# Kernel optimization log

Measured on AMD Instinct MI355X. Metric: run time of the kernel, lower is better.

The kernel has to match this reference:

```python
import jax, jax.numpy as jnp
import numpy as np

NU, B, N, D = 3, 16, 1024, 256  # n_utils, batch, tokens per util, embed dim


def l2norm(x, axis=-1, eps=1e-12):
    # F.normalize over channel dim: x / max(||x||_2, eps)
    n = jnp.linalg.norm(x, axis=axis, keepdims=True)
    return x / jnp.maximum(n, eps)


def setup_inputs() -> dict:
    key = jax.random.key(0)
    ks = jax.random.split(key, 20)
    s = 0.05
    return {
        "u0": jax.random.normal(ks[0], (B, N, D), jnp.float32),
        "u1": jax.random.normal(ks[1], (B, N, D), jnp.float32),
        "u2": jax.random.normal(ks[2], (B, N, D), jnp.float32),
        # Unary per util: embed Conv1d(D,D,1), feature_reduce Conv1d(D,1,1)
        "Wu": jax.random.normal(ks[3], (NU, D, D), jnp.float32) * s,
        "bu": jax.random.normal(ks[4], (NU, D), jnp.float32) * s,
        "wr": jax.random.normal(ks[5], (NU, D), jnp.float32) * s,
        "br": jax.random.normal(ks[6], (NU,), jnp.float32) * s,
        # Self Pairwise per util: embed_X, embed_Y Conv1d(D,D,1)
        "Wsx": jax.random.normal(ks[7], (NU, D, D), jnp.float32) * s,
        "bsx": jax.random.normal(ks[8], (NU, D), jnp.float32) * s,
        "Wsy": jax.random.normal(ks[9], (NU, D, D), jnp.float32) * s,
        "bsy": jax.random.normal(ks[10], (NU, D), jnp.float32) * s,
        # Cross Pairwise per ordered pair (i,j), i!=j (diagonal unused)
        "Wpx": jax.random.normal(ks[11], (NU, NU, D, D), jnp.float32) * s,
        "bpx": jax.random.normal(ks[12], (NU, NU, D), jnp.float32) * s,
        "Wpy": jax.random.normal(ks[13], (NU, NU, D, D), jnp.float32) * s,
        "bpy": jax.random.normal(ks[14], (NU, NU, D), jnp.float32) * s,
        # reduce_potentials: (i,i) -> Conv1d(4,1,1,bias=False); (i,j) -> Conv1d(3,1,1,bias=False)
        "wdiag": jax.random.normal(ks[15], (NU, 4), jnp.float32) * s,
        "wpair": jax.random.normal(ks[16], (NU, NU, 3), jnp.float32) * s,
    }


def _forward(u0, u1, u2, Wu, bu, wr, br, Wsx, bsx, Wsy, bsy,
             Wpx, bpx, Wpy, bpy, wdiag, wpair):
    U = jnp.stack([u0, u1, u2])  # (NU, b, n, d)

    # --- Unary potentials (eval mode: dropout = identity) ---
    Xe = jnp.einsum('ubnd,ued->ubne', U, Wu) + bu[:, None, None, :]
    unary = jnp.einsum('ubne,ue->ubn', jax.nn.relu(Xe), wr) + br[:, None, None]  # (NU,b,n)

    # --- Self Pairwise (x_spatial_dim=None path): embed, cosine-normalize over channels, affinity, mean ---
    Xs = l2norm(jnp.einsum('ubnd,ued->ubne', U, Wsx) + bsx[:, None, None, :])
    Ys = l2norm(jnp.einsum('ubnd,ued->ubne', U, Wsy) + bsy[:, None, None, :])
    S_self = jnp.einsum('ubne,ubme->ubnm', Xs, Ys)  # (NU,b,n,n)
    self_pot = S_self.mean(axis=3)                   # X_poten only (Y is None)  (NU,b,n)

    # --- Cross Pairwise over all ordered pairs (u,v) ---
    Xp = l2norm(jnp.einsum('ubnd,uved->uvbne', U, Wpx) + bpx[:, :, None, None, :])
    Yp = l2norm(jnp.einsum('vbnd,uved->uvbne', U, Wpy) + bpy[:, :, None, None, :])
    S = jnp.einsum('uvbne,uvbme->uvbnm', Xp, Yp)     # (NU,NU,b,n,n)
    pot_x = S.mean(axis=4)  # poten for util u in pair (u,v): (NU,NU,b,n)
    pot_y = S.mean(axis=3)  # poten for util v in pair (u,v): (NU,NU,b,n)

    # --- Reduce potentials per (target i, source j), softmax-attend over source tokens ---
    rows = []
    for i in range(NU):
        row = []
        for j in range(NU):
            if i == j:
                pots = [unary[i], self_pot[i]] + [pot_x[i, k] for k in range(NU) if k != i]
                w = wdiag[i]            # (4,)
            else:
                pots = [unary[j], self_pot[j], pot_y[i, j]]
                w = wpair[i, j]         # (3,)
            P = jnp.stack(pots, axis=1)                 # (b, k, n)
            red = jnp.einsum('bkn,k->bn', P, w)         # Conv1d(k,1,1,bias=False)
            a = jax.nn.softmax(red, axis=1)             # (b, n)
            row.append(jnp.einsum('bnd,bn->bd', U[j], a))  # attended feature (b, d)
        rows.append(jnp.stack(row))
    return jnp.stack(rows)  # (NU, NU, b, d)


def reference(u0, u1, u2, Wu, bu, wr, br, Wsx, bsx, Wsy, bsy,
              Wpx, bpx, Wpy, bpy, wdiag, wpair):
    return _forward(u0, u1, u2, Wu, bu, wr, br, Wsx, bsx, Wsy, bsy,
                    Wpx, bpx, Wpy, bpy, wdiag, wpair)
```

## Files before the change

### kernel.cpp

```cpp
#include <hip/hip_runtime.h>
#include <math.h>

#define NU 3
#define BB 16
#define NN 1024
#define DD 256
#define MM (BB*NN)
#define NPAIR 6

#define OFF_UNARY  0
#define OFF_INVXS  (OFF_UNARY + NU*MM)
#define OFF_INVXP  (OFF_INVXS + NU*MM)
#define OFF_INVYP  (OFF_INVXP + NPAIR*MM)
#define OFF_YBAR   (OFF_INVYP + NPAIR*MM)
#define OFF_XPBAR  (OFF_YBAR + NU*BB*DD)
#define OFF_YPBAR  (OFF_XPBAR + NPAIR*BB*DD)
#define OFF_PROJS  (OFF_YPBAR + NPAIR*BB*DD)
#define OFF_PROJX  (OFF_PROJS + NU*BB*DD)
#define OFF_PROJY  (OFF_PROJX + NPAIR*BB*DD)
#define OFF_CSS    (OFF_PROJY + NPAIR*BB*DD)
#define OFF_CSX    (OFF_CSS + NU*BB)
#define OFF_CSY    (OFF_CSX + NPAIR*BB)
#define OFF_SELFP  (OFF_CSY + NPAIR*BB)
#define OFF_POTX   (OFF_SELFP + NU*MM)
#define OFF_POTY   (OFF_POTX + NPAIR*MM)
#define WS_FLOATS  (OFF_POTY + NPAIR*MM)
#define OFF_PROB   (WS_FLOATS + 21*32768)
#define OFF_PART   (OFF_PROB + 9*BB*NN)

typedef _Float16 half8 __attribute__((ext_vector_type(8)));
typedef float f32x4 __attribute__((ext_vector_type(4)));

__device__ __forceinline__ const float* selU(int u, const float* u0, const float* u1, const float* u2) {
    return u == 0 ? u0 : (u == 1 ? u1 : u2);
}
__device__ __forceinline__ half8 cvt8(float4 a, float4 b) {
    half8 h = { (_Float16)a.x,(_Float16)a.y,(_Float16)a.z,(_Float16)a.w,
                (_Float16)b.x,(_Float16)b.y,(_Float16)b.z,(_Float16)b.w };
    return h;
}

__global__ __launch_bounds__(256) void convw_kernel(
    const float* __restrict__ Wu, const float* __restrict__ Wsx, const float* __restrict__ Wsy,
    const float* __restrict__ Wpx, const float* __restrict__ Wpy, float* __restrict__ ws)
{
    const int slot = blockIdx.x;
    const int kc   = blockIdx.y;
    const int tid  = threadIdx.x;
    const int u = slot / 7, s = slot % 7;
    const int j0 = (u==0)?1:0, j1 = (u==2)?1:2;
    const float* W =
        s==0 ? Wu  + (size_t)u*DD*DD :
        s==1 ? Wsx + (size_t)u*DD*DD :
        s==2 ? Wsy + (size_t)u*DD*DD :
        s==3 ? Wpx + (size_t)(u*NU+j0)*DD*DD :
        s==4 ? Wpx + (size_t)(u*NU+j1)*DD*DD :
        s==5 ? Wpy + (size_t)(j0*NU+u)*DD*DD :
               Wpy + (size_t)(j1*NU+u)*DD*DD;
    _Float16* wh = (_Float16*)(ws + WS_FLOATS) + (size_t)slot*65536;
    #pragma unroll
    for (int g = 0; g < 4; ++g) {
        const int idx16 = g*256 + tid;
        const int et   = idx16 >> 6;
        const int lane = idx16 & 63;
        const int e  = et*16 + (lane & 15);
        const int k0 = kc*32 + (lane >> 4)*8;
        const float* sp = W + (size_t)e*DD + k0;
        const float4 v0 = *reinterpret_cast<const float4*>(sp);
        const float4 v1 = *reinterpret_cast<const float4*>(sp + 4);
        *reinterpret_cast<half8*>(wh + ((size_t)(et*8 + kc)*64 + lane)*8) = cvt8(v0, v1);
    }
}

__global__ __launch_bounds__(256, 3) void pass1_kernel(
    const float* __restrict__ u0, const float* __restrict__ u1, const float* __restrict__ u2,
    const float* __restrict__ bu, const float* __restrict__ wr, const float* __restrict__ br,
    const float* __restrict__ bsx, const float* __restrict__ bsy,
    const float* __restrict__ bpx, const float* __restrict__ bpy,
    float* __restrict__ ws)
{
    __shared__ __align__(16) _Float16 Ub[16384];
    __shared__ float ep_sum[4][64];
    __shared__ float ep_inv[64];

    const int tid  = threadIdx.x;
    const int u    = blockIdx.y;
    const int row0 = blockIdx.x * 64;
    const int b    = row0 >> 10;

    const int j0 = (u==0)?1:0, j1 = (u==2)?1:2;
    const int px0 = u*2, px1 = u*2+1;
    const int py0 = (u==0)?2:((u==1)?0:1);
    const int py1 = (u==0)?4:((u==1)?5:3);

    const float* src = selU(u,u0,u1,u2);
    const _Float16* whU = (const _Float16*)(ws + WS_FLOATS) + (size_t)u*7*65536;

    const int lane = tid & 63, wq = tid >> 6;
    const int l15 = lane & 15, lg = lane >> 4;
    const int swz = (l15 >> 1) & 3;
    const int kxor = (lg ^ swz) * 8;

    const _Float16* wbase = whU + (size_t)wq*16384 + (size_t)lane*8;

    f32x4 acc[4][4];
    #pragma unroll
    for (int m = 0; m < 4; ++m)
        #pragma unroll
        for (int n = 0; n < 4; ++n) acc[m][n] = (f32x4)0.f;

    half8 bfA[4], bfB[4];
    half8 af_res[2][8];

#define BFLD(DST, S, KC) { \
    _Pragma("unroll") \
    for (int n_ = 0; n_ < 4; ++n_) \
        DST[n_] = *reinterpret_cast<const half8*>(wbase + (size_t)(S)*65536 + n_*4096 + (KC)*512); }

#define SLAB(KC, BFC, BFN) { \
    if ((KC) < 7) { BFLD(BFN, s, (KC)+1) } else if (s < 6) { BFLD(BFN, s+1, 0) } \
    half8 afd0 = *reinterpret_cast<const half8*>(&Ub[(KC)*2048 + (32 + l15)*32 + kxor]); \
    half8 afd1 = *reinterpret_cast<const half8*>(&Ub[(KC)*2048 + (48 + l15)*32 + kxor]); \
    _Pragma("unroll") \
    for (int n_ = 0; n_ < 4; ++n_) { \
        acc[0][n_] = __builtin_amdgcn_mfma_f32_16x16x32_f16(af_res[0][KC], BFC[n_], acc[0][n_],0,0,0); \
        acc[1][n_] = __builtin_amdgcn_mfma_f32_16x16x32_f16(af_res[1][KC], BFC[n_], acc[1][n_],0,0,0); } \
    _Pragma("unroll") \
    for (int n_ = 0; n_ < 4; ++n_) { \
        acc[2][n_] = __builtin_amdgcn_mfma_f32_16x16x32_f16(afd0, BFC[n_], acc[2][n_],0,0,0); \
        acc[3][n_] = __builtin_amdgcn_mfma_f32_16x16x32_f16(afd1, BFC[n_], acc[3][n_],0,0,0); } }

    BFLD(bfA, 0, 0)

    #pragma unroll
    for (int c = 0; c < 8; ++c) {
        const int G2 = c*256 + tid;
        const int t  = G2 >> 5;
        const int gk = G2 & 31;
        const int kc = gk >> 2, kg = gk & 3;
        const float* p = src + (size_t)(row0 + t)*DD + gk*8;
        const float4 v0 = *reinterpret_cast<const float4*>(p);
        const float4 v1 = *reinterpret_cast<const float4*>(p + 4);
        const int kgs = kg ^ ((t >> 1) & 3);
        *reinterpret_cast<half8*>(&Ub[kc*2048 + t*32 + kgs*8]) = cvt8(v0, v1);
    }
    __syncthreads();

    #pragma unroll
    for (int kc = 0; kc < 8; ++kc) {
        af_res[0][kc] = *reinterpret_cast<const half8*>(&Ub[kc*2048 + (l15)*32 + kxor]);
        af_res[1][kc] = *reinterpret_cast<const half8*>(&Ub[kc*2048 + (16 + l15)*32 + kxor]);
    }

    for (int s = 0; s < 7; ++s) {
        SLAB(0, bfA, bfB)
        SLAB(1, bfB, bfA)
        SLAB(2, bfA, bfB)
        SLAB(3, bfB, bfA)
        SLAB(4, bfA, bfB)
        SLAB(5, bfB, bfA)
        SLAB(6, bfA, bfB)
        SLAB(7, bfB, bfA)

        const float* bias =
            s==0 ? bu  + u*DD :
            s==1 ? bsx + u*DD :
            s==2 ? bsy + u*DD :
            s==3 ? bpx + (u*NU+j0)*DD :
            s==4 ? bpx + (u*NU+j1)*DD :
            s==5 ? bpy + (j0*NU+u)*DD :
                   bpy + (j1*NU+u)*DD;
        float bv[4];
        #pragma unroll
        for (int n = 0; n < 4; ++n) bv[n] = bias[wq*64 + n*16 + l15];
        #pragma unroll
        for (int m = 0; m < 4; ++m)
            #pragma unroll
            for (int n = 0; n < 4; ++n)
                #pragma unroll
                for (int r = 0; r < 4; ++r) acc[m][n][r] += bv[n];

        if (s == 0) {
            float wrv[4];
            #pragma unroll
            for (int n = 0; n < 4; ++n) wrv[n] = wr[u*DD + wq*64 + n*16 + l15];
            float pm[4][4];
            #pragma unroll
            for (int m = 0; m < 4; ++m)
                #pragma unroll
                for (int r = 0; r < 4; ++r) {
                    float t = 0.f;
                    #pragma unroll
                    for (int n = 0; n < 4; ++n) t = fmaf(fmaxf(acc[m][n][r], 0.f), wrv[n], t);
                    pm[m][r] = t;
                }
            #pragma unroll
            for (int mask = 1; mask <= 8; mask <<= 1)
                #pragma unroll
                for (int m = 0; m < 4; ++m)
                    #pragma unroll
                    for (int r = 0; r < 4; ++r) pm[m][r] += __shfl_xor(pm[m][r], mask);
            if (l15 == 0) {
                #pragma unroll
                for (int m = 0; m < 4; ++m)
                    #pragma unroll
                    for (int r = 0; r < 4; ++r) ep_sum[wq][m*16 + lg*4 + r] = pm[m][r];
            }
            __syncthreads();
            if (tid < 64)
                ws[OFF_UNARY + (size_t)u*MM + row0 + tid] =
                    ep_sum[0][tid]+ep_sum[1][tid]+ep_sum[2][tid]+ep_sum[3][tid] + br[u];
        } else {
            float pm[4][4];
            #pragma unroll
            for (int m = 0; m < 4; ++m)
                #pragma unroll
                for (int r = 0; r < 4; ++r) {
                    float t = 0.f;
                    #pragma unroll
                    for (int n = 0; n < 4; ++n) t = fmaf(acc[m][n][r], acc[m][n][r], t);
                    pm[m][r] = t;
                }
            #pragma unroll
            for (int mask = 1; mask <= 8; mask <<= 1)
                #pragma unroll
                for (int m = 0; m < 4; ++m)
                    #pragma unroll
                    for (int r = 0; r < 4; ++r) pm[m][r] += __shfl_xor(pm[m][r], mask);
            if (l15 == 0) {
                #pragma unroll
                for (int m = 0; m < 4; ++m)
                    #pragma unroll
                    for (int r = 0; r < 4; ++r) ep_sum[wq][m*16 + lg*4 + r] = pm[m][r];
            }
            __syncthreads();
            if (tid < 64) {
                const float ssum = ep_sum[0][tid]+ep_sum[1][tid]+ep_sum[2][tid]+ep_sum[3][tid];
                const float inv = 1.f / fmaxf(sqrtf(ssum), 1e-12f);
                ep_inv[tid] = inv;
                if (s == 1)      ws[OFF_INVXS + (size_t)u  *MM + row0 + tid] = inv;
                else if (s == 3) ws[OFF_INVXP + (size_t)px0*MM + row0 + tid] = inv;
                else if (s == 4) ws[OFF_INVXP + (size_t)px1*MM + row0 + tid] = inv;
                else if (s == 5) ws[OFF_INVYP + (size_t)py0*MM + row0 + tid] = inv;
                else if (s == 6) ws[OFF_INVYP + (size_t)py1*MM + row0 + tid] = inv;
            }
            __syncthreads();
            if (s >= 2) {
                float invv[4][4];
                #pragma unroll
                for (int m = 0; m < 4; ++m)
                    #pragma unroll
                    for (int r = 0; r < 4; ++r) invv[m][r] = ep_inv[m*16 + lg*4 + r];
                float qn[4];
                #pragma unroll
                for (int n = 0; n < 4; ++n) {
                    float t = 0.f;
                    #pragma unroll
                    for (int m = 0; m < 4; ++m)
                        #pragma unroll
                        for (int r = 0; r < 4; ++r) t = fmaf(acc[m][n][r], invv[m][r], t);
                    qn[n] = t;
                }
                #pragma unroll
                for (int n = 0; n < 4; ++n) {
                    qn[n] += __shfl_xor(qn[n], 16);
                    qn[n] += __shfl_xor(qn[n], 32);
                }
                float* bar =
                    s==2 ? ws + OFF_YBAR  + ((size_t)u  *BB + b)*DD :
                    s==3 ? ws + OFF_XPBAR + ((size_t)px0*BB + b)*DD :
                    s==4 ? ws + OFF_XPBAR + ((size_t)px1*BB + b)*DD :
                    s==5 ? ws + OFF_YPBAR + ((size_t)py0*BB + b)*DD :
                           ws + OFF_YPBAR + ((size_t)py1*BB + b)*DD;
                if (lane < 16) {
                    #pragma unroll
                    for (int n = 0; n < 4; ++n)
                        atomicAdd(&bar[wq*64 + n*16 + lane], qn[n]);
                }
            }
        }
        #pragma unroll
        for (int m = 0; m < 4; ++m)
            #pragma unroll
            for (int n = 0; n < 4; ++n) acc[m][n] = (f32x4)0.f;
        __syncthreads();
    }
#undef BFLD
#undef SLAB
}

__global__ __launch_bounds__(256) void proj_kernel(
    const float* __restrict__ Wsx, const float* __restrict__ bsx,
    const float* __restrict__ Wpx, const float* __restrict__ bpx,
    const float* __restrict__ Wpy, const float* __restrict__ bpy,
    float* __restrict__ ws)
{
    __shared__ float barl[DD];
    __shared__ float redl[256];
    const int task = blockIdx.x >> 4;
    const int b    = blockIdx.x & 15;
    const int tid  = threadIdx.x;
    const float *W, *bias, *barp;
    float *projp, *csp;
    if (task < 3) {
        const int uu = task;
        W = Wsx + (size_t)uu*DD*DD; bias = bsx + uu*DD;
        barp  = ws + OFF_YBAR  + ((size_t)uu*BB + b)*DD;
        projp = ws + OFF_PROJS + ((size_t)uu*BB + b)*DD;
        csp   = ws + OFF_CSS + uu*BB + b;
    } else if (task < 9) {
        const int p = task - 3; const int i = p>>1;
        const int j = (p&1) == 0 ? (i==0?1:0) : (i==2?1:2);
        W = Wpx + (size_t)(i*NU+j)*DD*DD; bias = bpx + (i*NU+j)*DD;
        barp  = ws + OFF_YPBAR + ((size_t)p*BB + b)*DD;
        projp = ws + OFF_PROJX + ((size_t)p*BB + b)*DD;
        csp   = ws + OFF_CSX + p*BB + b;
    } else {
        const int p = task - 9; const int i = p>>1;
        const int j = (p&1) == 0 ? (i==0?1:0) : (i==2?1:2);
        W = Wpy + (size_t)(i*NU+j)*DD*DD; bias = bpy + (i*NU+j)*DD;
        barp  = ws + OFF_XPBAR + ((size_t)p*BB + b)*DD;
        projp = ws + OFF_PROJY + ((size_t)p*BB + b)*DD;
        csp   = ws + OFF_CSY + p*BB + b;
    }
    barl[tid] = barp[tid] * (1.f / NN);
    __syncthreads();
    float s = 0.f;
    for (int e = 0; e < DD; ++e) s = fmaf(W[(size_t)e*DD + tid], barl[e], s);
    projp[tid] = s;
    redl[tid] = bias[tid] * barl[tid];
    __syncthreads();
    for (int st = 128; st > 0; st >>= 1) {
        if (tid < st) redl[tid] += redl[tid + st];
        __syncthreads();
    }
    if (tid == 0) *csp = redl[0];
}

__global__ __launch_bounds__(256) void pots_kernel(
    const float* __restrict__ u0, const float* __restrict__ u1, const float* __restrict__ u2,
    float* __restrict__ ws)
{
    __shared__ float projl[5][DD];
    __shared__ float csl[5];
    const int u    = blockIdx.y;
    const int row0 = blockIdx.x * 32;
    const int b    = row0 >> 10;
    const int tid  = threadIdx.x;
    const int px0 = u*2, px1 = u*2+1;
    const int py0 = (u==0)?2:((u==1)?0:1);
    const int py1 = (u==0)?4:((u==1)?5:3);

    projl[0][tid] = ws[OFF_PROJS + ((size_t)u  *BB + b)*DD + tid];
    projl[1][tid] = ws[OFF_PROJX + ((size_t)px0*BB + b)*DD + tid];
    projl[2][tid] = ws[OFF_PROJX + ((size_t)px1*BB + b)*DD + tid];
    projl[3][tid] = ws[OFF_PROJY + ((size_t)py0*BB + b)*DD + tid];
    projl[4][tid] = ws[OFF_PROJY + ((size_t)py1*BB + b)*DD + tid];
    if (tid == 0) {
        csl[0] = ws[OFF_CSS + u*BB + b];
        csl[1] = ws[OFF_CSX + px0*BB + b];
        csl[2] = ws[OFF_CSX + px1*BB + b];
        csl[3] = ws[OFF_CSY + py0*BB + b];
        csl[4] = ws[OFF_CSY + py1*BB + b];
    }
    __syncthreads();
    const float* src = selU(u,u0,u1,u2);
    const int token = tid >> 3, q = tid & 7;
    const int row = row0 + token;
    float a0=0.f,a1=0.f,a2=0.f,a3=0.f,a4=0.f;
    #pragma unroll
    for (int cc = 0; cc < 8; ++cc) {
        const int d0 = q*32 + cc*4;
        const float4 v  = *reinterpret_cast<const float4*>(src + (size_t)row*DD + d0);
        const float4 p0 = *reinterpret_cast<const float4*>(&projl[0][d0]);
        const float4 p1 = *reinterpret_cast<const float4*>(&projl[1][d0]);
        const float4 p2 = *reinterpret_cast<const float4*>(&projl[2][d0]);
        const float4 p3 = *reinterpret_cast<const float4*>(&projl[3][d0]);
        const float4 p4 = *reinterpret_cast<const float4*>(&projl[4][d0]);
        a0 = fmaf(v.x,p0.x,fmaf(v.y,p0.y,fmaf(v.z,p0.z,fmaf(v.w,p0.w,a0))));
        a1 = fmaf(v.x,p1.x,fmaf(v.y,p1.y,fmaf(v.z,p1.z,fmaf(v.w,p1.w,a1))));
        a2 = fmaf(v.x,p2.x,fmaf(v.y,p2.y,fmaf(v.z,p2.z,fmaf(v.w,p2.w,a2))));
        a3 = fmaf(v.x,p3.x,fmaf(v.y,p3.y,fmaf(v.z,p3.z,fmaf(v.w,p3.w,a3))));
        a4 = fmaf(v.x,p4.x,fmaf(v.y,p4.y,fmaf(v.z,p4.z,fmaf(v.w,p4.w,a4))));
    }
    #pragma unroll
    for (int mask = 1; mask <= 4; mask <<= 1) {
        a0 += __shfl_xor(a0, mask, 8);
        a1 += __shfl_xor(a1, mask, 8);
        a2 += __shfl_xor(a2, mask, 8);
        a3 += __shfl_xor(a3, mask, 8);
        a4 += __shfl_xor(a4, mask, 8);
    }
    if (q == 0) {
        ws[OFF_SELFP + (size_t)u  *MM + row] = (a0 + csl[0]) * ws[OFF_INVXS + (size_t)u  *MM + row];
        ws[OFF_POTX  + (size_t)px0*MM + row] = (a1 + csl[1]) * ws[OFF_INVXP + (size_t)px0*MM + row];
        ws[OFF_POTX  + (size_t)px1*MM + row] = (a2 + csl[2]) * ws[OFF_INVXP + (size_t)px1*MM + row];
        ws[OFF_POTY  + (size_t)py0*MM + row] = (a3 + csl[3]) * ws[OFF_INVYP + (size_t)py0*MM + row];
        ws[OFF_POTY  + (size_t)py1*MM + row] = (a4 + csl[4]) * ws[OFF_INVYP + (size_t)py1*MM + row];
    }
}

__global__ __launch_bounds__(256) void attend_logits_kernel(
    const float* __restrict__ wdiag, const float* __restrict__ wpair,
    float* __restrict__ ws)
{
    __shared__ float el[3][NN];
    __shared__ float redl[256];
    const int c = blockIdx.x;
    const int j = c >> 4, b = c & 15;
    const int tid = threadIdx.x;

    #pragma unroll
    for (int i = 0; i < 3; ++i) {
        if (i == j) {
            const int p1 = i*2, p2 = i*2+1;
            const float w0 = wdiag[i*4+0], w1 = wdiag[i*4+1], w2 = wdiag[i*4+2], w3 = wdiag[i*4+3];
            for (int n = tid; n < NN; n += 256) {
                const int row = b*NN + n;
                el[i][n] = w0*ws[OFF_UNARY + i*MM + row] + w1*ws[OFF_SELFP + i*MM + row]
                         + w2*ws[OFF_POTX + p1*MM + row] + w3*ws[OFF_POTX + p2*MM + row];
            }
        } else {
            const int p = i*2 + (j > i ? j-1 : j);
            const float w0 = wpair[(i*3+j)*3+0], w1 = wpair[(i*3+j)*3+1], w2 = wpair[(i*3+j)*3+2];
            for (int n = tid; n < NN; n += 256) {
                const int row = b*NN + n;
                el[i][n] = w0*ws[OFF_UNARY + j*MM + row] + w1*ws[OFF_SELFP + j*MM + row]
                         + w2*ws[OFF_POTY + p*MM + row];
            }
        }
    }
    __syncthreads();
    #pragma unroll
    for (int i = 0; i < 3; ++i) {
        float m = -1e30f;
        for (int n = tid; n < NN; n += 256) m = fmaxf(m, el[i][n]);
        redl[tid] = m; __syncthreads();
        for (int st = 128; st > 0; st >>= 1) {
            if (tid < st) redl[tid] = fmaxf(redl[tid], redl[tid+st]);
            __syncthreads();
        }
        m = redl[0];
        __syncthreads();
        float ss = 0.f;
        for (int n = tid; n < NN; n += 256) {
            const float e = expf(el[i][n] - m);
            el[i][n] = e;
            ss += e;
        }
        redl[tid] = ss; __syncthreads();
        for (int st = 128; st > 0; st >>= 1) {
            if (tid < st) redl[tid] += redl[tid+st];
            __syncthreads();
        }
        const float invS = 1.f / redl[0];
        __syncthreads();
        for (int n = tid; n < NN; n += 256)
            ws[OFF_PROB + ((size_t)(i*3+j)*BB + b)*NN + n] = el[i][n] * invS;
    }
}

__global__ __launch_bounds__(256) void attend_sum_kernel(
    const float* __restrict__ u0, const float* __restrict__ u1, const float* __restrict__ u2,
    const float* __restrict__ ws, float* __restrict__ wso)
{
    __shared__ float pl[3][128];
    const int x  = blockIdx.x;
    const int jb = x >> 3, ch = x & 7;
    const int j = jb >> 4, b = jb & 15;
    const int tid = threadIdx.x;

    for (int t = tid; t < 384; t += 256) {
        const int i = t >> 7, n = t & 127;
        pl[i][n] = ws[OFF_PROB + ((size_t)(i*3+j)*BB + b)*NN + ch*128 + n];
    }
    __syncthreads();
    const float* Uj = selU(j, u0, u1, u2) + ((size_t)b*NN + ch*128)*DD;
    float a0 = 0.f, a1 = 0.f, a2 = 0.f;
    #pragma unroll 4
    for (int n = 0; n < 128; ++n) {
        const float v = Uj[(size_t)n*DD + tid];
        a0 = fmaf(pl[0][n], v, a0);
        a1 = fmaf(pl[1][n], v, a1);
        a2 = fmaf(pl[2][n], v, a2);
    }
    wso[OFF_PART + (((size_t)(0*3+j)*BB + b)*8 + ch)*DD + tid] = a0;
    wso[OFF_PART + (((size_t)(1*3+j)*BB + b)*8 + ch)*DD + tid] = a1;
    wso[OFF_PART + (((size_t)(2*3+j)*BB + b)*8 + ch)*DD + tid] = a2;
}

__global__ __launch_bounds__(256) void attend_reduce_kernel(
    const float* __restrict__ ws, float* __restrict__ out)
{
    const int ijb = blockIdx.x;
    const int tid = threadIdx.x;
    float s = 0.f;
    #pragma unroll
    for (int ch = 0; ch < 8; ++ch)
        s += ws[OFF_PART + ((size_t)ijb*8 + ch)*DD + tid];
    out[(size_t)ijb*DD + tid] = s;
}

extern "C" void kernel_launch(void* const* d_in, const int* in_sizes, int n_in,
                              void* d_out, int out_size, void* d_ws, size_t ws_size,
                              hipStream_t stream)
{
    (void)in_sizes; (void)n_in; (void)out_size; (void)ws_size;
    const float* u0    = (const float*)d_in[0];
    const float* u1    = (const float*)d_in[1];
    const float* u2    = (const float*)d_in[2];
    const float* Wu    = (const float*)d_in[3];
    const float* bu    = (const float*)d_in[4];
    const float* wr    = (const float*)d_in[5];
    const float* br    = (const float*)d_in[6];
    const float* Wsx   = (const float*)d_in[7];
    const float* bsx   = (const float*)d_in[8];
    const float* Wsy   = (const float*)d_in[9];
    const float* bsy   = (const float*)d_in[10];
    const float* Wpx   = (const float*)d_in[11];
    const float* bpx   = (const float*)d_in[12];
    const float* Wpy   = (const float*)d_in[13];
    const float* bpy   = (const float*)d_in[14];
    const float* wdiag = (const float*)d_in[15];
    const float* wpair = (const float*)d_in[16];
    float* ws  = (float*)d_ws;
    float* out = (float*)d_out;

    hipMemsetAsync(ws + OFF_YBAR, 0, (size_t)(NU + 2*NPAIR)*BB*DD*sizeof(float), stream);

    dim3 gw(21, 8);
    convw_kernel<<<gw, 256, 0, stream>>>(Wu, Wsx, Wsy, Wpx, Wpy, ws);

    dim3 g1(MM/64, 3);
    pass1_kernel<<<g1, 256, 0, stream>>>(u0,u1,u2,bu,wr,br,bsx,bsy,bpx,bpy,ws);

    proj_kernel<<<15*BB, 256, 0, stream>>>(Wsx,bsx,Wpx,bpx,Wpy,bpy,ws);
    dim3 g2(MM/32, 3);
    pots_kernel<<<g2, 256, 0, stream>>>(u0,u1,u2,ws);

    attend_logits_kernel<<<3*BB, 256, 0, stream>>>(wdiag, wpair, ws);
    attend_sum_kernel<<<3*BB*8, 256, 0, stream>>>(u0,u1,u2, ws, ws);
    attend_reduce_kernel<<<9*BB, 256, 0, stream>>>(ws, out);
}
```

Measured before the change: 142.1 us.

## Map pass1 tiles to XCDs by util and deepen weight prefetch to two slabs

Replaces the 2D grid of pass1 with a 1D grid of 784 blocks. Block id modulo 8 picks an XCD, and each XCD is given mostly tiles of a single util's weight set, so those fp16 weights stay resident in that XCD's L2 instead of being pulled into every cache. It also raises the register prefetch of weight fragments from one slab ahead to two, using four rotating buffers, to hide more global load latency. The costs are extra VGPRs, which could hurt occupancy under launch_bounds(256,3), and a hardcoded round-robin assumption about how blocks are dispatched to XCDs, with some padding blocks that exit immediately.

```diff
diff --git a/kernel.cpp b/kernel.cpp
--- a/kernel.cpp
+++ b/kernel.cpp
@@ -83,9 +83,24 @@
     __shared__ float ep_sum[4][64];
     __shared__ float ep_inv[64];
 
-    const int tid  = threadIdx.x;
-    const int u    = blockIdx.y;
-    const int row0 = blockIdx.x * 64;
+    const int tid = threadIdx.x;
+
+    const int bid  = blockIdx.x;
+    const int xcd  = bid & 7;
+    const int slot = bid >> 3;
+    int u, tile;
+    if (xcd < 6) {
+        const int g   = (xcd < 3) ? xcd : xcd - 3;
+        const int uo  = (xcd < 3) ? 0 : 1;
+        const int cnt = (g == 2) ? 84 : 86;
+        if (slot < cnt)           { u = uo; tile = g*86 + slot; }
+        else if (slot < cnt + 10) { u = 2;  tile = xcd*10 + (slot - cnt); }
+        else return;
+    } else {
+        if (slot >= 98) return;
+        u = 2; tile = 60 + (xcd - 6)*98 + slot;
+    }
+    const int row0 = tile * 64;
     const int b    = row0 >> 10;
 
     const int j0 = (u==0)?1:0, j1 = (u==2)?1:2;
@@ -109,7 +124,7 @@
         #pragma unroll
         for (int n = 0; n < 4; ++n) acc[m][n] = (f32x4)0.f;
 
-    half8 bfA[4], bfB[4];
+    half8 bf0[4], bf1[4], bf2[4], bf3[4];
     half8 af_res[2][8];
 
 #define BFLD(DST, S, KC) { \
@@ -117,8 +132,8 @@
     for (int n_ = 0; n_ < 4; ++n_) \
         DST[n_] = *reinterpret_cast<const half8*>(wbase + (size_t)(S)*65536 + n_*4096 + (KC)*512); }
 
-#define SLAB(KC, BFC, BFN) { \
-    if ((KC) < 7) { BFLD(BFN, s, (KC)+1) } else if (s < 6) { BFLD(BFN, s+1, 0) } \
+#define SLAB(KC, BFC, ISSB, ISS_S, ISS_KC) { \
+    if ((ISS_S) < 7) { BFLD(ISSB, (ISS_S), (ISS_KC)) } \
     half8 afd0 = *reinterpret_cast<const half8*>(&Ub[(KC)*2048 + (32 + l15)*32 + kxor]); \
     half8 afd1 = *reinterpret_cast<const half8*>(&Ub[(KC)*2048 + (48 + l15)*32 + kxor]); \
     _Pragma("unroll") \
@@ -130,7 +145,8 @@
         acc[2][n_] = __builtin_amdgcn_mfma_f32_16x16x32_f16(afd0, BFC[n_], acc[2][n_],0,0,0); \
         acc[3][n_] = __builtin_amdgcn_mfma_f32_16x16x32_f16(afd1, BFC[n_], acc[3][n_],0,0,0); } }
 
-    BFLD(bfA, 0, 0)
+    BFLD(bf0, 0, 0)
+    BFLD(bf1, 0, 1)
 
     #pragma unroll
     for (int c = 0; c < 8; ++c) {
@@ -153,14 +169,14 @@
     }
 
     for (int s = 0; s < 7; ++s) {
-        SLAB(0, bfA, bfB)
-        SLAB(1, bfB, bfA)
-        SLAB(2, bfA, bfB)
-        SLAB(3, bfB, bfA)
-        SLAB(4, bfA, bfB)
-        SLAB(5, bfB, bfA)
-        SLAB(6, bfA, bfB)
-        SLAB(7, bfB, bfA)
+        SLAB(0, bf0, bf2, s,   2)
+        SLAB(1, bf1, bf3, s,   3)
+        SLAB(2, bf2, bf0, s,   4)
+        SLAB(3, bf3, bf1, s,   5)
+        SLAB(4, bf0, bf2, s,   6)
+        SLAB(5, bf1, bf3, s,   7)
+        SLAB(6, bf2, bf0, s+1, 0)
+        SLAB(7, bf3, bf1, s+1, 1)
 
         const float* bias =
             s==0 ? bu  + u*DD :
@@ -531,8 +547,7 @@
     dim3 gw(21, 8);
     convw_kernel<<<gw, 256, 0, stream>>>(Wu, Wsx, Wsy, Wpx, Wpy, ws);
 
-    dim3 g1(MM/64, 3);
-    pass1_kernel<<<g1, 256, 0, stream>>>(u0,u1,u2,bu,wr,br,bsx,bsy,bpx,bpy,ws);
+    pass1_kernel<<<784, 256, 0, stream>>>(u0,u1,u2,bu,wr,br,bsx,bsy,bpx,bpy,ws);
 
     proj_kernel<<<15*BB, 256, 0, stream>>>(Wsx,bsx,Wpx,bpx,Wpy,bpy,ws);
     dim3 g2(MM/32, 3);
```

New measurement: 185.5 us. 1.3x slower.
